# Performance work log

Measured on AMD Instinct MI355X. Metric: run time of the kernel, lower is better.

Reference implementation:

```python
import jax, jax.numpy as jnp
import numpy as np

N_NODES = 50000
N_EDGES = 800000
IN_CH = 64
HID = 128
OUT_AGE, OUT_SEX, OUT_ETH = 21, 2, 5


def _glorot(key, shape):
    fan_in, fan_out = shape
    lim = float(np.sqrt(6.0 / (fan_in + fan_out)))
    return jax.random.uniform(key, shape, jnp.float32, -lim, lim)


def sage_conv(x, src, dst, Wl, Wr, b, n_nodes):
    # PyG SAGEConv (mean aggr): out = lin_l(mean_{j->i} x_j) + lin_r(x_i) + bias
    msg_sum = jax.ops.segment_sum(x[src], dst, num_segments=n_nodes)  # [N, d]
    deg = jax.ops.segment_sum(jnp.ones((src.shape[0],), x.dtype), dst,
                              num_segments=n_nodes)  # [N]
    mean = msg_sum / jnp.maximum(deg, 1.0)[:, None]
    return mean @ Wl + x @ Wr + b


def setup_inputs() -> dict:
    key = jax.random.key(0)
    ks = jax.random.split(key, 16)
    x = jax.random.normal(ks[0], (N_NODES, IN_CH), jnp.float32)
    edge_src = jax.random.randint(ks[1], (N_EDGES,), 0, N_NODES)
    edge_dst = jax.random.randint(ks[2], (N_EDGES,), 0, N_NODES)
    dims = [(IN_CH, HID), (HID, HID), (HID, HID),
            (HID, OUT_AGE), (HID, OUT_SEX), (HID, OUT_ETH)]
    names = ['1', '2', '3', 'age', 'sex', 'eth']
    inp = {'x': x, 'edge_src': edge_src, 'edge_dst': edge_dst}
    for i, (nm, (di, do)) in enumerate(zip(names, dims)):
        inp[f'Wl_{nm}'] = _glorot(ks[3 + 2 * i], (di, do))
        inp[f'Wr_{nm}'] = _glorot(ks[4 + 2 * i], (di, do))
        inp[f'b_{nm}'] = jnp.zeros((do,), jnp.float32)
    return inp


def reference(x, edge_src, edge_dst,
              Wl_1, Wr_1, b_1, Wl_2, Wr_2, b_2, Wl_3, Wr_3, b_3,
              Wl_age, Wr_age, b_age, Wl_sex, Wr_sex, b_sex,
              Wl_eth, Wr_eth, b_eth):
    n = x.shape[0]
    h = jax.nn.relu(sage_conv(x, edge_src, edge_dst, Wl_1, Wr_1, b_1, n))
    h = jax.nn.relu(sage_conv(h, edge_src, edge_dst, Wl_2, Wr_2, b_2, n))
    h = jax.nn.relu(sage_conv(h, edge_src, edge_dst, Wl_3, Wr_3, b_3, n))
    age = sage_conv(h, edge_src, edge_dst, Wl_age, Wr_age, b_age, n)
    sex = sage_conv(h, edge_src, edge_dst, Wl_sex, Wr_sex, b_sex, n)
    eth = sage_conv(h, edge_src, edge_dst, Wl_eth, Wr_eth, b_eth, n)
    return (age, sex, eth)
```

## Files before the change

### kernel.cpp

```cpp
#include <hip/hip_runtime.h>
#include <hip/hip_bf16.h>


typedef __attribute__((ext_vector_type(8))) short bf16x8;
typedef __attribute__((ext_vector_type(4))) float f32x4;

#define NBSH 7
#define EPW  4096

__device__ __forceinline__ unsigned short f2b(float f) {
    __hip_bfloat16 h = __float2bfloat16(f);
    return *reinterpret_cast<unsigned short*>(&h);
}
__device__ __forceinline__ float b2f(unsigned short u) {
    __hip_bfloat16 h;
    *reinterpret_cast<unsigned short*>(&h) = u;
    return __bfloat162float(h);
}

__global__ void bucket_hist(const int* __restrict__ dst, int* __restrict__ ghist,
                            int n_edges, int nb) {
    __shared__ int lh[512];
    int tid = threadIdx.x;
    for (int i = tid; i < 512; i += 256) lh[i] = 0;
    __syncthreads();
    int stride = gridDim.x * blockDim.x;
    for (int e = blockIdx.x * blockDim.x + tid; e < n_edges; e += stride)
        atomicAdd(&lh[dst[e] >> NBSH], 1);
    __syncthreads();
    for (int i = tid; i < nb; i += 256)
        if (lh[i]) atomicAdd(&ghist[i], lh[i]);
}

__global__ void scan_buckets(const int* __restrict__ hist, int* __restrict__ base,
                             int* __restrict__ cur, int nb, int n_edges) {
    __shared__ int tmp[512];
    int t = threadIdx.x;
    int v = (t < nb) ? hist[t] : 0;
    tmp[t] = v;
    __syncthreads();
    for (int off = 1; off < 512; off <<= 1) {
        int u = (t >= off) ? tmp[t - off] : 0;
        __syncthreads();
        tmp[t] += u;
        __syncthreads();
    }
    if (t < nb) {
        base[t] = tmp[t] - v;
        cur[t] = tmp[t] - v;
    }
    if (t == 0) base[nb] = n_edges;
}

__global__ __launch_bounds__(512) void bin_edges_lds(
    const int* __restrict__ src, const int* __restrict__ dst,
    int* __restrict__ bkt_cur, uint2* __restrict__ ebuf, int n_edges, int nb) {
    __shared__ int hist[512];
    __shared__ int hbase[513];
    __shared__ int hcur[512];
    __shared__ uint2 sorted[EPW];
    int tid = threadIdx.x;
    int chunk0 = blockIdx.x * EPW;
    int cnt = min(EPW, n_edges - chunk0);
    hist[tid] = 0;
    __syncthreads();
    for (int i = tid; i < cnt; i += 512) atomicAdd(&hist[dst[chunk0 + i] >> NBSH], 1);
    __syncthreads();
    int v = hist[tid];
    hbase[tid] = v;
    __syncthreads();
    for (int off = 1; off < 512; off <<= 1) {
        int u = (tid >= off) ? hbase[tid - off] : 0;
        __syncthreads();
        hbase[tid] += u;
        __syncthreads();
    }
    int excl = hbase[tid] - v;
    __syncthreads();
    hbase[tid] = excl;
    hcur[tid] = excl;
    if (tid == 511) hbase[512] = excl + v;
    __syncthreads();
    for (int i = tid; i < cnt; i += 512) {
        int s = src[chunk0 + i];
        int d = dst[chunk0 + i];
        int p = atomicAdd(&hcur[d >> NBSH], 1);
        sorted[p] = make_uint2((unsigned)s, (unsigned)d);
    }
    __syncthreads();
    int cntb = hbase[tid + 1] - hbase[tid];
    int gb = 0;
    if (tid < nb && cntb > 0) gb = atomicAdd(&bkt_cur[tid], cntb);
    hist[tid] = gb;
    __syncthreads();
    for (int i = tid; i < cnt; i += 512) {
        uint2 ed = sorted[i];
        int b = (int)(ed.y >> NBSH);
        ebuf[hist[b] + (i - hbase[b])] = ed;
    }
}

__global__ void sort_bucket(const uint2* __restrict__ ebuf, const int* __restrict__ bkt_base,
                            int* __restrict__ row_start, int* __restrict__ col,
                            int n_nodes, int n_edges) {
    __shared__ int hist[128];
    __shared__ int sc[128];
    __shared__ int hcur[128];
    int b = blockIdx.x, tid = threadIdx.x;
    int lo = b << NBSH;
    if (tid < 128) hist[tid] = 0;
    __syncthreads();
    int s = bkt_base[b], t = bkt_base[b + 1];
    for (int i = s + tid; i < t; i += 256) atomicAdd(&hist[(int)ebuf[i].y - lo], 1);
    __syncthreads();
    if (tid < 128) sc[tid] = hist[tid];
    __syncthreads();
    for (int off = 1; off < 128; off <<= 1) {
        int u = (tid < 128 && tid >= off) ? sc[tid - off] : 0;
        __syncthreads();
        if (tid < 128) sc[tid] += u;
        __syncthreads();
    }
    if (tid < 128) {
        int excl = sc[tid] - hist[tid];
        hcur[tid] = excl;
        int node = lo + tid;
        if (node < n_nodes) row_start[node] = s + excl;
    }
    if (b == 0 && tid == 0) row_start[n_nodes] = n_edges;
    __syncthreads();
    for (int i = s + tid; i < t; i += 256) {
        uint2 ed = ebuf[i];
        int p = atomicAdd(&hcur[(int)ed.y - lo], 1);
        col[s + p] = (int)ed.x;
    }
}

__device__ __forceinline__ void bt_body(const float* __restrict__ Wl,
                                        const float* __restrict__ Wr,
                                        unsigned short* __restrict__ Bt,
                                        int KA, int idx) {
    int KTOT = 2 * KA;
    if (idx >= 128 * KTOT) return;
    int n = idx / KTOT, k = idx % KTOT;
    float v = (k < KA) ? Wl[k * 128 + n] : Wr[(k - KA) * 128 + n];
    Bt[idx] = f2b(v);
}

__global__ void prep_all(const float* __restrict__ x, unsigned short* __restrict__ xb, int n4,
                         const float* __restrict__ Wl1, const float* __restrict__ Wr1,
                         unsigned short* __restrict__ Bt1,
                         const float* __restrict__ Wl2, const float* __restrict__ Wr2,
                         unsigned short* __restrict__ Bt2,
                         const float* __restrict__ Wl3, const float* __restrict__ Wr3,
                         unsigned short* __restrict__ Bt3,
                         const float* __restrict__ Wl_age, const float* __restrict__ Wl_sex,
                         const float* __restrict__ Wl_eth,
                         const float* __restrict__ Wr_age, const float* __restrict__ Wr_sex,
                         const float* __restrict__ Wr_eth,
                         const float* __restrict__ b_age, const float* __restrict__ b_sex,
                         const float* __restrict__ b_eth,
                         float* __restrict__ Wl_cat, float* __restrict__ Wr_cat,
                         float* __restrict__ b_cat, int* __restrict__ bkt_hist) {
    int nbx = (n4 + 255) / 256;
    int b = blockIdx.x;
    if (b < nbx) {
        int t = b * 256 + threadIdx.x;
        if (t < n4) {
            float4 v = reinterpret_cast<const float4*>(x)[t];
            uint2 o;
            o.x = (unsigned)f2b(v.x) | ((unsigned)f2b(v.y) << 16);
            o.y = (unsigned)f2b(v.z) | ((unsigned)f2b(v.w) << 16);
            reinterpret_cast<uint2*>(xb)[t] = o;
        }
        return;
    }
    b -= nbx;
    if (b < 64)  { bt_body(Wl1, Wr1, Bt1, 64,  b * 256 + threadIdx.x); return; }
    b -= 64;
    if (b < 128) { bt_body(Wl2, Wr2, Bt2, 128, b * 256 + threadIdx.x); return; }
    b -= 128;
    if (b < 128) { bt_body(Wl3, Wr3, Bt3, 128, b * 256 + threadIdx.x); return; }
    b -= 128;
    if (b < 14) {
        int idx = b * 256 + threadIdx.x;
        if (idx < 128 * 28) {
            int k = idx / 28, j = idx % 28;
            float vl, vr;
            if (j < 21) {
                vl = Wl_age[k * 21 + j];
                vr = Wr_age[k * 21 + j];
            } else if (j < 23) {
                vl = Wl_sex[k * 2 + (j - 21)];
                vr = Wr_sex[k * 2 + (j - 21)];
            } else {
                vl = Wl_eth[k * 5 + (j - 23)];
                vr = Wr_eth[k * 5 + (j - 23)];
            }
            Wl_cat[idx] = vl;
            Wr_cat[idx] = vr;
        }
        if (idx < 28)
            b_cat[idx] = (idx < 21) ? b_age[idx] : (idx < 23) ? b_sex[idx - 21] : b_eth[idx - 23];
        return;
    }
    bkt_hist[threadIdx.x] = 0;
    bkt_hist[256 + threadIdx.x] = 0;
}

__global__ void agg128_bf(const unsigned short* __restrict__ feat,
                          const int* __restrict__ row_start, const int* __restrict__ col,
                          unsigned short* __restrict__ mean, int n_nodes) {
    int wave = (blockIdx.x * blockDim.x + threadIdx.x) >> 6;
    int lane = threadIdx.x & 63;
    if (wave >= n_nodes) return;
    int s0 = row_start[wave];
    int deg = row_start[wave + 1] - s0;
    const unsigned* f2 = reinterpret_cast<const unsigned*>(feat);
    float a0 = 0.f, a1 = 0.f, b0 = 0.f, b1 = 0.f;
    float c0 = 0.f, c1 = 0.f, d0 = 0.f, d1 = 0.f;
    for (int base = 0; base < deg; base += 64) {
        int blk = min(64, deg - base);
        int cv = col[s0 + base + min(lane, blk - 1)];
        int i = 0;
        for (; i + 3 < blk; i += 4) {
            int e0 = __shfl(cv, i), e1 = __shfl(cv, i + 1);
            int e2 = __shfl(cv, i + 2), e3 = __shfl(cv, i + 3);
            unsigned u0 = f2[(size_t)e0 * 64 + lane];
            unsigned u1 = f2[(size_t)e1 * 64 + lane];
            unsigned u2 = f2[(size_t)e2 * 64 + lane];
            unsigned u3 = f2[(size_t)e3 * 64 + lane];
            a0 += b2f((unsigned short)(u0 & 0xffff)); a1 += b2f((unsigned short)(u0 >> 16));
            b0 += b2f((unsigned short)(u1 & 0xffff)); b1 += b2f((unsigned short)(u1 >> 16));
            c0 += b2f((unsigned short)(u2 & 0xffff)); c1 += b2f((unsigned short)(u2 >> 16));
            d0 += b2f((unsigned short)(u3 & 0xffff)); d1 += b2f((unsigned short)(u3 >> 16));
        }
        for (; i < blk; ++i) {
            int e0 = __shfl(cv, i);
            unsigned u0 = f2[(size_t)e0 * 64 + lane];
            a0 += b2f((unsigned short)(u0 & 0xffff)); a1 += b2f((unsigned short)(u0 >> 16));
        }
    }
    float inv = (deg > 0) ? 1.0f / (float)deg : 0.0f;
    float sA = (a0 + b0) + (c0 + d0);
    float sB = (a1 + b1) + (c1 + d1);
    unsigned o = (unsigned)f2b(sA * inv) | ((unsigned)f2b(sB * inv) << 16);
    reinterpret_cast<unsigned*>(mean)[(size_t)wave * 64 + lane] = o;
}

__global__ void agg64_bf(const unsigned short* __restrict__ feat,
                         const int* __restrict__ row_start, const int* __restrict__ col,
                         unsigned short* __restrict__ mean, int n_nodes) {
    int wave = (blockIdx.x * blockDim.x + threadIdx.x) >> 6;
    int lane = threadIdx.x & 63;
    if (wave >= n_nodes) return;
    int half = lane >> 5;
    int lp = lane & 31;
    int s0 = row_start[wave];
    int deg = row_start[wave + 1] - s0;
    const unsigned* f2 = reinterpret_cast<const unsigned*>(feat);
    float a0 = 0.f, a1 = 0.f, b0 = 0.f, b1 = 0.f;
    float c0 = 0.f, c1 = 0.f, d0 = 0.f, d1 = 0.f;
    for (int base = 0; base < deg; base += 64) {
        int blk = min(64, deg - base);
        int cv = col[s0 + base + min(lane, blk - 1)];
        int nfull = blk & ~7;
        for (int i = half * 4; i < nfull; i += 8) {
            int e0 = __shfl(cv, i), e1 = __shfl(cv, i + 1);
            int e2 = __shfl(cv, i + 2), e3 = __shfl(cv, i + 3);
            unsigned u0 = f2[(size_t)e0 * 32 + lp];
            unsigned u1 = f2[(size_t)e1 * 32 + lp];
            unsigned u2 = f2[(size_t)e2 * 32 + lp];
            unsigned u3 = f2[(size_t)e3 * 32 + lp];
            a0 += b2f((unsigned short)(u0 & 0xffff)); a1 += b2f((unsigned short)(u0 >> 16));
            b0 += b2f((unsigned short)(u1 & 0xffff)); b1 += b2f((unsigned short)(u1 >> 16));
            c0 += b2f((unsigned short)(u2 & 0xffff)); c1 += b2f((unsigned short)(u2 >> 16));
            d0 += b2f((unsigned short)(u3 & 0xffff)); d1 += b2f((unsigned short)(u3 >> 16));
        }
        int tstart = nfull + half * 4;
        int tend = min(blk, tstart + 4);
        for (int i = tstart; i < tend; ++i) {
            int e0 = __shfl(cv, i);
            unsigned u0 = f2[(size_t)e0 * 32 + lp];
            a0 += b2f((unsigned short)(u0 & 0xffff)); a1 += b2f((unsigned short)(u0 >> 16));
        }
    }
    float sA = (a0 + b0) + (c0 + d0);
    float sB = (a1 + b1) + (c1 + d1);
    sA += __shfl_down(sA, 32);
    sB += __shfl_down(sB, 32);
    if (half == 0) {
        float inv = (deg > 0) ? 1.0f / (float)deg : 0.0f;
        unsigned o = (unsigned)f2b(sA * inv) | ((unsigned)f2b(sB * inv) << 16);
        reinterpret_cast<unsigned*>(mean)[(size_t)wave * 32 + lp] = o;
    }
}

template <int KTOT, int KA>
__global__ __launch_bounds__(256) void mfma_layer(
    const unsigned short* __restrict__ A0, const unsigned short* __restrict__ A1,
    const unsigned short* __restrict__ Bt, const float* __restrict__ bias,
    unsigned short* __restrict__ out, int n_nodes) {
    constexpr int KC = KTOT / 64;
    __shared__ __align__(16) unsigned short sA[64][72];
    __shared__ __align__(16) unsigned short sB[128][72];
    int node0 = blockIdx.x * 64;
    int tid = threadIdx.x;
    int w = tid >> 6, lane = tid & 63;
    f32x4 acc[8] = {};
    for (int kc = 0; kc < KC; ++kc) {
        const unsigned short* Asrc;
        int kbase, aw;
        if (kc * 64 < KA) { Asrc = A0; kbase = kc * 64; aw = KA; }
        else              { Asrc = A1; kbase = kc * 64 - KA; aw = KTOT - KA; }
        {
            int nd = tid >> 2, k16 = (tid & 3) * 16;
            uint4 v0 = {0, 0, 0, 0}, v1 = {0, 0, 0, 0};
            int gn = node0 + nd;
            if (gn < n_nodes) {
                const uint4* src = reinterpret_cast<const uint4*>(Asrc + (size_t)gn * aw + kbase + k16);
                v0 = src[0];
                v1 = src[1];
            }
            uint4* dst = reinterpret_cast<uint4*>(&sA[nd][k16]);
            dst[0] = v0;
            dst[1] = v1;
        }
        {
            int n = tid >> 1, k32 = (tid & 1) * 32;
            const uint4* src = reinterpret_cast<const uint4*>(Bt + (size_t)n * KTOT + kc * 64 + k32);
            uint4* dst = reinterpret_cast<uint4*>(&sB[n][k32]);
            dst[0] = src[0];
            dst[1] = src[1];
            dst[2] = src[2];
            dst[3] = src[3];
        }
        __syncthreads();
#pragma unroll
        for (int ks = 0; ks < 2; ++ks) {
            int kl = ks * 32 + (lane >> 4) * 8;
            bf16x8 af = *reinterpret_cast<const bf16x8*>(&sA[w * 16 + (lane & 15)][kl]);
#pragma unroll
            for (int t = 0; t < 8; ++t) {
                bf16x8 bfr = *reinterpret_cast<const bf16x8*>(&sB[t * 16 + (lane & 15)][kl]);
                acc[t] = __builtin_amdgcn_mfma_f32_16x16x32_bf16(af, bfr, acc[t], 0, 0, 0);
            }
        }
        __syncthreads();
    }
    int r0 = w * 16, cq = lane >> 4, cr = lane & 15;
#pragma unroll
    for (int t = 0; t < 8; ++t) {
        int colj = t * 16 + cr;
        float bv = bias[colj];
#pragma unroll
        for (int i = 0; i < 4; ++i) {
            int node = node0 + r0 + cq * 4 + i;
            if (node < n_nodes) {
                float v = fmaxf(acc[t][i] + bv, 0.0f);
                out[(size_t)node * 128 + colj] = f2b(v);
            }
        }
    }
}

__global__ __launch_bounds__(256) void proj2_kernel(
    const unsigned short* __restrict__ h,
    const float* __restrict__ Wl_cat, const float* __restrict__ Wr_cat,
    const float* __restrict__ b_cat,
    float* __restrict__ p, float* __restrict__ q, int n_nodes) {
    __shared__ float sh[64][128];
    __shared__ float swl[128 * 28];
    __shared__ float swr[128 * 28];
    int node0 = blockIdx.x * 64;
    int tid = threadIdx.x;
    for (int i = tid; i < 128 * 28; i += 256) {
        swl[i] = Wl_cat[i];
        swr[i] = Wr_cat[i];
    }
    for (int it = tid; it < 1024; it += 256) {
        int n = it >> 4, k8 = (it & 15) * 8;
        int node = node0 + n;
        if (node < n_nodes) {
            uint4 u = *reinterpret_cast<const uint4*>(h + (size_t)node * 128 + k8);
            sh[n][k8 + 0] = b2f((unsigned short)(u.x & 0xffff));
            sh[n][k8 + 1] = b2f((unsigned short)(u.x >> 16));
            sh[n][k8 + 2] = b2f((unsigned short)(u.y & 0xffff));
            sh[n][k8 + 3] = b2f((unsigned short)(u.y >> 16));
            sh[n][k8 + 4] = b2f((unsigned short)(u.z & 0xffff));
            sh[n][k8 + 5] = b2f((unsigned short)(u.z >> 16));
            sh[n][k8 + 6] = b2f((unsigned short)(u.w & 0xffff));
            sh[n][k8 + 7] = b2f((unsigned short)(u.w >> 16));
        } else {
            for (int z = 0; z < 8; ++z) sh[n][k8 + z] = 0.f;
        }
    }
    __syncthreads();
    int j = tid & 31, ng = tid >> 5;
    float accp[8] = {};
    float accq[8] = {};
    if (j < 28) {
        for (int k = 0; k < 128; k += 2) {
            float wl0 = swl[k * 28 + j],       wr0 = swr[k * 28 + j];
            float wl1 = swl[(k + 1) * 28 + j], wr1 = swr[(k + 1) * 28 + j];
#pragma unroll
            for (int i = 0; i < 8; ++i) {
                float2 hv = *reinterpret_cast<const float2*>(&sh[ng * 8 + i][k]);
                accp[i] += hv.x * wl0 + hv.y * wl1;
                accq[i] += hv.x * wr0 + hv.y * wr1;
            }
        }
    }
    float bj = (j < 28) ? b_cat[j] : 0.f;
#pragma unroll
    for (int i = 0; i < 8; ++i) {
        int node = node0 + ng * 8 + i;
        if (node < n_nodes) {
            p[(size_t)node * 32 + j] = (j < 28) ? accp[i] : 0.f;
            q[(size_t)node * 32 + j] = (j < 28) ? (accq[i] + bj) : 0.f;
        }
    }
}

__global__ void head_final(const float* __restrict__ p, const float* __restrict__ q,
                           const int* __restrict__ row_start, const int* __restrict__ col,
                           float* __restrict__ age, float* __restrict__ sex,
                           float* __restrict__ eth, int n_nodes) {
    int node = (blockIdx.x * blockDim.x + threadIdx.x) >> 5;
    int lane = threadIdx.x & 63;
    int lp = lane & 31;
    int grpbase = lane & 32;
    if (node >= n_nodes) return;
    int s0 = row_start[node];
    int deg = row_start[node + 1] - s0;
    float a = 0.f, b = 0.f, c = 0.f, d = 0.f;
    for (int base = 0; base < deg; base += 32) {
        int blk = min(32, deg - base);
        int cv = col[s0 + base + min(lp, blk - 1)];
        int i = 0;
        for (; i + 3 < blk; i += 4) {
            int e0 = __shfl(cv, grpbase + i),     e1 = __shfl(cv, grpbase + i + 1);
            int e2 = __shfl(cv, grpbase + i + 2), e3 = __shfl(cv, grpbase + i + 3);
            a += p[(size_t)e0 * 32 + lp];
            b += p[(size_t)e1 * 32 + lp];
            c += p[(size_t)e2 * 32 + lp];
            d += p[(size_t)e3 * 32 + lp];
        }
        for (; i < blk; ++i) {
            int e0 = __shfl(cv, grpbase + i);
            a += p[(size_t)e0 * 32 + lp];
        }
    }
    float inv = (deg > 0) ? 1.0f / (float)deg : 0.0f;
    float out = ((a + b) + (c + d)) * inv + q[(size_t)node * 32 + lp];
    if (lp < 21)
        age[(size_t)node * 21 + lp] = out;
    else if (lp < 23)
        sex[(size_t)node * 2 + (lp - 21)] = out;
    else if (lp < 28)
        eth[(size_t)node * 5 + (lp - 23)] = out;
}

extern "C" void kernel_launch(void* const* d_in, const int* in_sizes, int n_in,
                              void* d_out, int out_size, void* d_ws, size_t ws_size,
                              hipStream_t stream) {
    const float* x        = (const float*)d_in[0];
    const int*   edge_src = (const int*)d_in[1];
    const int*   edge_dst = (const int*)d_in[2];
    const float* Wl_1 = (const float*)d_in[3];
    const float* Wr_1 = (const float*)d_in[4];
    const float* b_1  = (const float*)d_in[5];
    const float* Wl_2 = (const float*)d_in[6];
    const float* Wr_2 = (const float*)d_in[7];
    const float* b_2  = (const float*)d_in[8];
    const float* Wl_3 = (const float*)d_in[9];
    const float* Wr_3 = (const float*)d_in[10];
    const float* b_3  = (const float*)d_in[11];
    const float* Wl_age = (const float*)d_in[12];
    const float* Wr_age = (const float*)d_in[13];
    const float* b_age  = (const float*)d_in[14];
    const float* Wl_sex = (const float*)d_in[15];
    const float* Wr_sex = (const float*)d_in[16];
    const float* b_sex  = (const float*)d_in[17];
    const float* Wl_eth = (const float*)d_in[18];
    const float* Wr_eth = (const float*)d_in[19];
    const float* b_eth  = (const float*)d_in[20];

    const int n_nodes = in_sizes[0] / 64;
    const int n_edges = in_sizes[1];

    char* ws = (char*)d_ws;
    int*            row_start = (int*)(ws + 200192);
    int*            col       = (int*)(ws + 600576);
    unsigned short* Bt1       = (unsigned short*)(ws + 3800832);
    unsigned short* Bt2       = (unsigned short*)(ws + 3833600);
    unsigned short* Bt3       = (unsigned short*)(ws + 3899136);
    float*          Wl_cat    = (float*)(ws + 3964672);
    float*          Wr_cat    = (float*)(ws + 3979008);
    float*          b_cat     = (float*)(ws + 3993344);
    unsigned short* xb        = (unsigned short*)(ws + 3993600);
    unsigned short* h_bf      = (unsigned short*)(ws + 10393856);
    unsigned short* mean_bf   = (unsigned short*)(ws + 23194112);
    float*          p         = (float*)(ws + 35994368);
    float*          q         = (float*)(ws + 42394624);
    uint2*          ebuf      = (uint2*)p;
    int*            bkt_hist  = (int*)q;
    int*            bkt_base  = bkt_hist + 512;
    int*            bkt_cur   = bkt_hist + 1032;

    float* out_age = (float*)d_out;
    float* out_sex = out_age + (size_t)n_nodes * 21;
    float* out_eth = out_sex + (size_t)n_nodes * 2;

    const int nb      = (n_nodes + 127) >> NBSH;
    const int nchunks = (n_edges + EPW - 1) / EPW;
    const int n4      = n_nodes * 64 / 4;

    {
        int grid = (n4 + 255) / 256 + 64 + 128 + 128 + 14 + 1;
        prep_all<<<grid, 256, 0, stream>>>(
            x, xb, n4, Wl_1, Wr_1, Bt1, Wl_2, Wr_2, Bt2, Wl_3, Wr_3, Bt3,
            Wl_age, Wl_sex, Wl_eth, Wr_age, Wr_sex, Wr_eth, b_age, b_sex, b_eth,
            Wl_cat, Wr_cat, b_cat, bkt_hist);
    }

    bucket_hist<<<256, 256, 0, stream>>>(edge_dst, bkt_hist, n_edges, nb);
    scan_buckets<<<1, 512, 0, stream>>>(bkt_hist, bkt_base, bkt_cur, nb, n_edges);
    bin_edges_lds<<<nchunks, 512, 0, stream>>>(edge_src, edge_dst, bkt_cur, ebuf, n_edges, nb);
    sort_bucket<<<nb, 256, 0, stream>>>(ebuf, bkt_base, row_start, col, n_nodes, n_edges);

    const int agg_grid  = (n_nodes * 64 + 255) / 256;
    const int gemm_grid = (n_nodes + 63) / 64;

    agg64_bf<<<agg_grid, 256, 0, stream>>>(xb, row_start, col, mean_bf, n_nodes);
    mfma_layer<128, 64><<<gemm_grid, 256, 0, stream>>>(mean_bf, xb, Bt1, b_1, h_bf, n_nodes);

    agg128_bf<<<agg_grid, 256, 0, stream>>>(h_bf, row_start, col, mean_bf, n_nodes);
    mfma_layer<256, 128><<<gemm_grid, 256, 0, stream>>>(mean_bf, h_bf, Bt2, b_2, h_bf, n_nodes);

    agg128_bf<<<agg_grid, 256, 0, stream>>>(h_bf, row_start, col, mean_bf, n_nodes);
    mfma_layer<256, 128><<<gemm_grid, 256, 0, stream>>>(mean_bf, h_bf, Bt3, b_3, h_bf, n_nodes);

    proj2_kernel<<<(n_nodes + 63) / 64, 256, 0, stream>>>(h_bf, Wl_cat, Wr_cat, b_cat, p, q, n_nodes);
    head_final<<<(n_nodes * 32 + 255) / 256, 256, 0, stream>>>(
        p, q, row_start, col, out_age, out_sex, out_eth, n_nodes);
}
```

Baseline: 316.4 us.

## Fuse neighbor mean aggregation into the MFMA layer kernel via shared memory

Each SAGE layer's gather-mean aggregation now runs inside the GEMM kernel. Each wave aggregates 16 nodes into a shared-memory tile that feeds the MFMA directly, which removes the separate aggregation kernels and the global round-trip of the mean buffer. The price is a much smaller grid for the latency-bound gather (one block per 64 nodes, each wave handling 16 nodes in sequence), plus extra LDS that may cut occupancy. Ping-pong h buffers replace in-place writes, since other blocks still read neighbor features.

```diff
diff --git a/kernel.cpp b/kernel.cpp
--- a/kernel.cpp
+++ b/kernel.cpp
@@ -208,117 +208,108 @@
     bkt_hist[256 + threadIdx.x] = 0;
 }
 
-__global__ void agg128_bf(const unsigned short* __restrict__ feat,
-                          const int* __restrict__ row_start, const int* __restrict__ col,
-                          unsigned short* __restrict__ mean, int n_nodes) {
-    int wave = (blockIdx.x * blockDim.x + threadIdx.x) >> 6;
-    int lane = threadIdx.x & 63;
-    if (wave >= n_nodes) return;
-    int s0 = row_start[wave];
-    int deg = row_start[wave + 1] - s0;
-    const unsigned* f2 = reinterpret_cast<const unsigned*>(feat);
-    float a0 = 0.f, a1 = 0.f, b0 = 0.f, b1 = 0.f;
-    float c0 = 0.f, c1 = 0.f, d0 = 0.f, d1 = 0.f;
-    for (int base = 0; base < deg; base += 64) {
-        int blk = min(64, deg - base);
-        int cv = col[s0 + base + min(lane, blk - 1)];
-        int i = 0;
-        for (; i + 3 < blk; i += 4) {
-            int e0 = __shfl(cv, i), e1 = __shfl(cv, i + 1);
-            int e2 = __shfl(cv, i + 2), e3 = __shfl(cv, i + 3);
-            unsigned u0 = f2[(size_t)e0 * 64 + lane];
-            unsigned u1 = f2[(size_t)e1 * 64 + lane];
-            unsigned u2 = f2[(size_t)e2 * 64 + lane];
-            unsigned u3 = f2[(size_t)e3 * 64 + lane];
-            a0 += b2f((unsigned short)(u0 & 0xffff)); a1 += b2f((unsigned short)(u0 >> 16));
-            b0 += b2f((unsigned short)(u1 & 0xffff)); b1 += b2f((unsigned short)(u1 >> 16));
-            c0 += b2f((unsigned short)(u2 & 0xffff)); c1 += b2f((unsigned short)(u2 >> 16));
-            d0 += b2f((unsigned short)(u3 & 0xffff)); d1 += b2f((unsigned short)(u3 >> 16));
-        }
-        for (; i < blk; ++i) {
-            int e0 = __shfl(cv, i);
-            unsigned u0 = f2[(size_t)e0 * 64 + lane];
-            a0 += b2f((unsigned short)(u0 & 0xffff)); a1 += b2f((unsigned short)(u0 >> 16));
-        }
-    }
-    float inv = (deg > 0) ? 1.0f / (float)deg : 0.0f;
-    float sA = (a0 + b0) + (c0 + d0);
-    float sB = (a1 + b1) + (c1 + d1);
-    unsigned o = (unsigned)f2b(sA * inv) | ((unsigned)f2b(sB * inv) << 16);
-    reinterpret_cast<unsigned*>(mean)[(size_t)wave * 64 + lane] = o;
-}
-
-__global__ void agg64_bf(const unsigned short* __restrict__ feat,
-                         const int* __restrict__ row_start, const int* __restrict__ col,
-                         unsigned short* __restrict__ mean, int n_nodes) {
-    int wave = (blockIdx.x * blockDim.x + threadIdx.x) >> 6;
-    int lane = threadIdx.x & 63;
-    if (wave >= n_nodes) return;
-    int half = lane >> 5;
-    int lp = lane & 31;
-    int s0 = row_start[wave];
-    int deg = row_start[wave + 1] - s0;
-    const unsigned* f2 = reinterpret_cast<const unsigned*>(feat);
-    float a0 = 0.f, a1 = 0.f, b0 = 0.f, b1 = 0.f;
-    float c0 = 0.f, c1 = 0.f, d0 = 0.f, d1 = 0.f;
-    for (int base = 0; base < deg; base += 64) {
-        int blk = min(64, deg - base);
-        int cv = col[s0 + base + min(lane, blk - 1)];
-        int nfull = blk & ~7;
-        for (int i = half * 4; i < nfull; i += 8) {
-            int e0 = __shfl(cv, i), e1 = __shfl(cv, i + 1);
-            int e2 = __shfl(cv, i + 2), e3 = __shfl(cv, i + 3);
-            unsigned u0 = f2[(size_t)e0 * 32 + lp];
-            unsigned u1 = f2[(size_t)e1 * 32 + lp];
-            unsigned u2 = f2[(size_t)e2 * 32 + lp];
-            unsigned u3 = f2[(size_t)e3 * 32 + lp];
-            a0 += b2f((unsigned short)(u0 & 0xffff)); a1 += b2f((unsigned short)(u0 >> 16));
-            b0 += b2f((unsigned short)(u1 & 0xffff)); b1 += b2f((unsigned short)(u1 >> 16));
-            c0 += b2f((unsigned short)(u2 & 0xffff)); c1 += b2f((unsigned short)(u2 >> 16));
-            d0 += b2f((unsigned short)(u3 & 0xffff)); d1 += b2f((unsigned short)(u3 >> 16));
-        }
-        int tstart = nfull + half * 4;
-        int tend = min(blk, tstart + 4);
-        for (int i = tstart; i < tend; ++i) {
-            int e0 = __shfl(cv, i);
-            unsigned u0 = f2[(size_t)e0 * 32 + lp];
-            a0 += b2f((unsigned short)(u0 & 0xffff)); a1 += b2f((unsigned short)(u0 >> 16));
-        }
-    }
-    float sA = (a0 + b0) + (c0 + d0);
-    float sB = (a1 + b1) + (c1 + d1);
-    sA += __shfl_down(sA, 32);
-    sB += __shfl_down(sB, 32);
-    if (half == 0) {
-        float inv = (deg > 0) ? 1.0f / (float)deg : 0.0f;
-        unsigned o = (unsigned)f2b(sA * inv) | ((unsigned)f2b(sB * inv) << 16);
-        reinterpret_cast<unsigned*>(mean)[(size_t)wave * 32 + lp] = o;
-    }
-}
-
 template <int KTOT, int KA>
-__global__ __launch_bounds__(256) void mfma_layer(
-    const unsigned short* __restrict__ A0, const unsigned short* __restrict__ A1,
+__global__ __launch_bounds__(256) void layer_fused(
+    const unsigned short* __restrict__ feat,
+    const int* __restrict__ row_start, const int* __restrict__ col,
     const unsigned short* __restrict__ Bt, const float* __restrict__ bias,
     unsigned short* __restrict__ out, int n_nodes) {
     constexpr int KC = KTOT / 64;
     __shared__ __align__(16) unsigned short sA[64][72];
     __shared__ __align__(16) unsigned short sB[128][72];
+    __shared__ __align__(16) unsigned short sMean[64][KA + 8];
     int node0 = blockIdx.x * 64;
     int tid = threadIdx.x;
     int w = tid >> 6, lane = tid & 63;
+    const unsigned* f2 = reinterpret_cast<const unsigned*>(feat);
+
+    for (int nd = 0; nd < 16; ++nd) {
+        int node = node0 + w * 16 + nd;
+        if (node >= n_nodes) break;
+        int s0 = row_start[node];
+        int deg = row_start[node + 1] - s0;
+        unsigned* mrow = reinterpret_cast<unsigned*>(&sMean[w * 16 + nd][0]);
+        if (KA == 128) {
+            float a0 = 0.f, a1 = 0.f, b0 = 0.f, b1 = 0.f;
+            float c0 = 0.f, c1 = 0.f, d0 = 0.f, d1 = 0.f;
+            for (int base = 0; base < deg; base += 64) {
+                int blk = min(64, deg - base);
+                int cv = col[s0 + base + min(lane, blk - 1)];
+                int i = 0;
+                for (; i + 3 < blk; i += 4) {
+                    int e0 = __shfl(cv, i), e1 = __shfl(cv, i + 1);
+                    int e2 = __shfl(cv, i + 2), e3 = __shfl(cv, i + 3);
+                    unsigned u0 = f2[(size_t)e0 * 64 + lane];
+                    unsigned u1 = f2[(size_t)e1 * 64 + lane];
+                    unsigned u2 = f2[(size_t)e2 * 64 + lane];
+                    unsigned u3 = f2[(size_t)e3 * 64 + lane];
+                    a0 += b2f((unsigned short)(u0 & 0xffff)); a1 += b2f((unsigned short)(u0 >> 16));
+                    b0 += b2f((unsigned short)(u1 & 0xffff)); b1 += b2f((unsigned short)(u1 >> 16));
+                    c0 += b2f((unsigned short)(u2 & 0xffff)); c1 += b2f((unsigned short)(u2 >> 16));
+                    d0 += b2f((unsigned short)(u3 & 0xffff)); d1 += b2f((unsigned short)(u3 >> 16));
+                }
+                for (; i < blk; ++i) {
+                    int e0 = __shfl(cv, i);
+                    unsigned u0 = f2[(size_t)e0 * 64 + lane];
+                    a0 += b2f((unsigned short)(u0 & 0xffff)); a1 += b2f((unsigned short)(u0 >> 16));
+                }
+            }
+            float inv = (deg > 0) ? 1.0f / (float)deg : 0.0f;
+            float sAc = (a0 + b0) + (c0 + d0);
+            float sBc = (a1 + b1) + (c1 + d1);
+            mrow[lane] = (unsigned)f2b(sAc * inv) | ((unsigned)f2b(sBc * inv) << 16);
+        } else {
+            int half = lane >> 5;
+            int lp = lane & 31;
+            float a0 = 0.f, a1 = 0.f, b0 = 0.f, b1 = 0.f;
+            float c0 = 0.f, c1 = 0.f, d0 = 0.f, d1 = 0.f;
+            for (int base = 0; base < deg; base += 64) {
+                int blk = min(64, deg - base);
+                int cv = col[s0 + base + min(lane, blk - 1)];
+                int nfull = blk & ~7;
+                for (int i = half * 4; i < nfull; i += 8) {
+                    int e0 = __shfl(cv, i), e1 = __shfl(cv, i + 1);
+                    int e2 = __shfl(cv, i + 2), e3 = __shfl(cv, i + 3);
+                    unsigned u0 = f2[(size_t)e0 * 32 + lp];
+                    unsigned u1 = f2[(size_t)e1 * 32 + lp];
+                    unsigned u2 = f2[(size_t)e2 * 32 + lp];
+                    unsigned u3 = f2[(size_t)e3 * 32 + lp];
+                    a0 += b2f((unsigned short)(u0 & 0xffff)); a1 += b2f((unsigned short)(u0 >> 16));
+                    b0 += b2f((unsigned short)(u1 & 0xffff)); b1 += b2f((unsigned short)(u1 >> 16));
+                    c0 += b2f((unsigned short)(u2 & 0xffff)); c1 += b2f((unsigned short)(u2 >> 16));
+                    d0 += b2f((unsigned short)(u3 & 0xffff)); d1 += b2f((unsigned short)(u3 >> 16));
+                }
+                int tstart = nfull + half * 4;
+                int tend = min(blk, tstart + 4);
+                for (int i = tstart; i < tend; ++i) {
+                    int e0 = __shfl(cv, i);
+                    unsigned u0 = f2[(size_t)e0 * 32 + lp];
+                    a0 += b2f((unsigned short)(u0 & 0xffff)); a1 += b2f((unsigned short)(u0 >> 16));
+                }
+            }
+            float sAc = (a0 + b0) + (c0 + d0);
+            float sBc = (a1 + b1) + (c1 + d1);
+            sAc += __shfl_down(sAc, 32);
+            sBc += __shfl_down(sBc, 32);
+            if (half == 0) {
+                float inv = (deg > 0) ? 1.0f / (float)deg : 0.0f;
+                mrow[lp] = (unsigned)f2b(sAc * inv) | ((unsigned)f2b(sBc * inv) << 16);
+            }
+        }
+    }
+    __syncthreads();
+
     f32x4 acc[8] = {};
     for (int kc = 0; kc < KC; ++kc) {
-        const unsigned short* Asrc;
-        int kbase, aw;
-        if (kc * 64 < KA) { Asrc = A0; kbase = kc * 64; aw = KA; }
-        else              { Asrc = A1; kbase = kc * 64 - KA; aw = KTOT - KA; }
-        {
+        bool from_mean = (kc * 64 < KA);
+        if (!from_mean) {
+            constexpr int AW = KTOT - KA;
+            int kbase = kc * 64 - KA;
             int nd = tid >> 2, k16 = (tid & 3) * 16;
             uint4 v0 = {0, 0, 0, 0}, v1 = {0, 0, 0, 0};
             int gn = node0 + nd;
             if (gn < n_nodes) {
-                const uint4* src = reinterpret_cast<const uint4*>(Asrc + (size_t)gn * aw + kbase + k16);
+                const uint4* src = reinterpret_cast<const uint4*>(feat + (size_t)gn * AW + kbase + k16);
                 v0 = src[0];
                 v1 = src[1];
             }
@@ -339,7 +330,11 @@
 #pragma unroll
         for (int ks = 0; ks < 2; ++ks) {
             int kl = ks * 32 + (lane >> 4) * 8;
-            bf16x8 af = *reinterpret_cast<const bf16x8*>(&sA[w * 16 + (lane & 15)][kl]);
+            bf16x8 af;
+            if (from_mean)
+                af = *reinterpret_cast<const bf16x8*>(&sMean[w * 16 + (lane & 15)][kc * 64 + kl]);
+            else
+                af = *reinterpret_cast<const bf16x8*>(&sA[w * 16 + (lane & 15)][kl]);
 #pragma unroll
             for (int t = 0; t < 8; ++t) {
                 bf16x8 bfr = *reinterpret_cast<const bf16x8*>(&sB[t * 16 + (lane & 15)][kl]);
@@ -499,8 +494,8 @@
     float*          Wr_cat    = (float*)(ws + 3979008);
     float*          b_cat     = (float*)(ws + 3993344);
     unsigned short* xb        = (unsigned short*)(ws + 3993600);
-    unsigned short* h_bf      = (unsigned short*)(ws + 10393856);
-    unsigned short* mean_bf   = (unsigned short*)(ws + 23194112);
+    unsigned short* h0        = (unsigned short*)(ws + 10393856);
+    unsigned short* h1        = (unsigned short*)(ws + 23194112);
     float*          p         = (float*)(ws + 35994368);
     float*          q         = (float*)(ws + 42394624);
     uint2*          ebuf      = (uint2*)p;
@@ -529,19 +524,13 @@
     bin_edges_lds<<<nchunks, 512, 0, stream>>>(edge_src, edge_dst, bkt_cur, ebuf, n_edges, nb);
     sort_bucket<<<nb, 256, 0, stream>>>(ebuf, bkt_base, row_start, col, n_nodes, n_edges);
 
-    const int agg_grid  = (n_nodes * 64 + 255) / 256;
     const int gemm_grid = (n_nodes + 63) / 64;
 
-    agg64_bf<<<agg_grid, 256, 0, stream>>>(xb, row_start, col, mean_bf, n_nodes);
-    mfma_layer<128, 64><<<gemm_grid, 256, 0, stream>>>(mean_bf, xb, Bt1, b_1, h_bf, n_nodes);
-
-    agg128_bf<<<agg_grid, 256, 0, stream>>>(h_bf, row_start, col, mean_bf, n_nodes);
-    mfma_layer<256, 128><<<gemm_grid, 256, 0, stream>>>(mean_bf, h_bf, Bt2, b_2, h_bf, n_nodes);
-
-    agg128_bf<<<agg_grid, 256, 0, stream>>>(h_bf, row_start, col, mean_bf, n_nodes);
-    mfma_layer<256, 128><<<gemm_grid, 256, 0, stream>>>(mean_bf, h_bf, Bt3, b_3, h_bf, n_nodes);
-
-    proj2_kernel<<<(n_nodes + 63) / 64, 256, 0, stream>>>(h_bf, Wl_cat, Wr_cat, b_cat, p, q, n_nodes);
+    layer_fused<128, 64><<<gemm_grid, 256, 0, stream>>>(xb, row_start, col, Bt1, b_1, h0, n_nodes);
+    layer_fused<256, 128><<<gemm_grid, 256, 0, stream>>>(h0, row_start, col, Bt2, b_2, h1, n_nodes);
+    layer_fused<256, 128><<<gemm_grid, 256, 0, stream>>>(h1, row_start, col, Bt3, b_3, h0, n_nodes);
+
+    proj2_kernel<<<(n_nodes + 63) / 64, 256, 0, stream>>>(h0, Wl_cat, Wr_cat, b_cat, p, q, n_nodes);
     head_final<<<(n_nodes * 32 + 255) / 256, 256, 0, stream>>>(
         p, q, row_start, col, out_age, out_sex, out_eth, n_nodes);
 }
```

Result: slower. 447.9 us (+41.5%).
